# Performance work log

Hardware: AMD Instinct MI355X
Metric: run time of the kernel (lower is better)

The kernel has to match this reference:

```python
import jax, jax.numpy as jnp
import numpy as np

WD, WH, WW = 7, 7, 7  # 3D window size


def _relative_position_index():
    # Matches the torch buffer construction exactly.
    coords = np.stack(np.meshgrid(np.arange(WD), np.arange(WH), np.arange(WW), indexing='ij'))  # [3,wd,wh,ww]
    cf = coords.reshape(3, -1)                      # [3, n]
    rel = cf[:, :, None] - cf[:, None, :]           # [3, n, n]
    rel = rel.transpose(1, 2, 0).copy()             # [n, n, 3]
    rel[..., 0] += WD - 1
    rel[..., 1] += WH - 1
    rel[..., 2] += WW - 1
    rel[..., 0] *= (2 * WH - 1) * (2 * WW - 1)
    rel[..., 1] *= (2 * WW - 1)
    return rel.sum(-1).astype(np.int32)             # [n, n] in [0, 2197)


def setup_inputs() -> dict:
    key = jax.random.key(0)
    ks = jax.random.split(key, 10)
    DIM, H = 192, 6
    B, N, NW = 256, WD * WH * WW, 64  # b = batch*num_windows, NW divides B
    TABLE = (2 * WD - 1) * (2 * WH - 1) * (2 * WW - 1)  # 2197
    w_std = 0.02
    mask = jnp.where(jax.random.uniform(ks[2], (NW, N, N)) < 0.1, -100.0, 0.0).astype(jnp.float32)
    return {
        'x_q': jax.random.normal(ks[0], (B, N, DIM), jnp.float32),
        'x_kv': jax.random.normal(ks[1], (B, N, DIM), jnp.float32),
        'mask': mask,
        'q_w': jax.random.normal(ks[3], (DIM, DIM), jnp.float32) * w_std,
        'q_b': jnp.zeros((DIM,), jnp.float32),
        'kv_w': jax.random.normal(ks[4], (2 * DIM, DIM), jnp.float32) * w_std,
        'kv_b': jnp.zeros((2 * DIM,), jnp.float32),
        'proj_w': jax.random.normal(ks[5], (DIM, DIM), jnp.float32) * w_std,
        'proj_b': jnp.zeros((DIM,), jnp.float32),
        'rpb_table': jax.random.normal(ks[6], (TABLE, H), jnp.float32) * w_std,
        'rpi': jnp.asarray(_relative_position_index()),
    }


def reference(x_q, x_kv, mask, q_w, q_b, kv_w, kv_b, proj_w, proj_b, rpb_table, rpi):
    b, n, c = x_q.shape
    h = rpb_table.shape[-1]
    d = c // h
    scale = d ** (-0.5)
    # projections (torch Linear: y = x @ W.T + b)
    q = (x_q @ q_w.T + q_b).reshape(b, n, h, d)
    kv = x_kv @ kv_w.T + kv_b                      # [b, n, 2c]
    k = kv[..., :c].reshape(b, n, h, d)
    v = kv[..., c:].reshape(b, n, h, d)
    # windowed QK^T
    attn = jnp.einsum('bnhd,bmhd->bhnm', q * scale, k)  # [b, h, n, n]
    # gathered relative-position bias
    rpb = rpb_table[rpi[:n, :n].reshape(-1)].reshape(n, n, h).transpose(2, 0, 1)  # [h, n, n]
    attn = attn + rpb[None]
    # window mask add
    nw = mask.shape[0]
    attn = attn.reshape(b // nw, nw, h, n, n) + mask[None, :, None]
    attn = jax.nn.softmax(attn.reshape(b, h, n, n), axis=-1)
    out = jnp.einsum('bhnm,bmhd->bnhd', attn, v).reshape(b, n, c)
    return out @ proj_w.T + proj_b
```

## Files before the change

kernel.cpp:

```cpp
#include <hip/hip_runtime.h>
#include <hip/hip_bf16.h>
#include <cstdint>

#define B_    256
#define N_    343
#define C_    192
#define H_    6
#define D_    32
#define NW_   64
#define M_    (B_*N_)
#define NN_   (N_*N_)
#define VTS_  352
#define RPS_  344
#define SCALE_ 0.17677669529663687f
#define LOG2E_ 1.4426950408889634f
#define SCALE_LOG2E_ (SCALE_ * LOG2E_)

typedef unsigned short ushort_t;
typedef __attribute__((ext_vector_type(8))) short short8;
typedef __attribute__((ext_vector_type(4))) float f32x4;
typedef __attribute__((ext_vector_type(16))) float f32x16;

__device__ __forceinline__ float b2f(unsigned int u) {
    return __uint_as_float(u << 16);
}
__device__ __forceinline__ unsigned int f2b(float f) {
    unsigned int x = __float_as_uint(f);
    x += 0x7FFFu + ((x >> 16) & 1u);
    return x >> 16;
}
__device__ __forceinline__ unsigned int cvt_pk(float a, float b) {
    unsigned int r;
    asm("v_cvt_pk_bf16_f32 %0, %1, %2" : "=v"(r) : "v"(a), "v"(b));
    return r;
}
__device__ __forceinline__ void pswap(unsigned int &x, unsigned int &y) {
    asm("v_permlane32_swap_b32 %0, %1" : "+v"(x), "+v"(y));
}

__global__ __launch_bounds__(256) void wcvt(
    const float* __restrict__ qw, const float* __restrict__ kvw,
    const float* __restrict__ pw, ushort_t* __restrict__ wb)
{
    int i = blockIdx.x * 256 + threadIdx.x;
    if (i >= 36864) return;
    float4 v;
    if (i < 9216)       v = ((const float4*)qw)[i];
    else if (i < 27648) v = ((const float4*)kvw)[i - 9216];
    else                v = ((const float4*)pw)[i - 27648];
    uint2 u;
    u.x = cvt_pk(v.x, v.y);
    u.y = cvt_pk(v.z, v.w);
    ((uint2*)wb)[i] = u;
}

__global__ __launch_bounds__(512, 4) void gemm_qkv(
    const float* __restrict__ xq, const float* __restrict__ xkv,
    const ushort_t* __restrict__ wb,
    const float* __restrict__ qbias, const float* __restrict__ kvbias,
    ushort_t* __restrict__ qx, ushort_t* __restrict__ kx,
    ushort_t* __restrict__ vtb)
{
    __shared__ ushort_t wls[192 * 200];

    const int t = threadIdx.x, wv = t >> 6, lane = t & 63;
    const int quad = lane >> 4, col = lane & 15;
    const int lid = blockIdx.x;
    const int xcd = lid & 7, idx = lid >> 3;
    const int wg = (xcd < 2 ? xcd * 258 : 2 * 258 + (xcd - 2) * 257) + idx;
    const int jsel = wg % 3;
    const int m0 = (wg / 3) * 128;
    const ushort_t* W = wb + (size_t)jsel * 36864;
    const float* Xf = (jsel == 0) ? xq : xkv;
    const float* bias = (jsel == 0) ? qbias : (jsel == 1 ? kvbias : kvbias + 192);
    const float alpha = (jsel == 0) ? SCALE_LOG2E_ : 1.0f;

    float4 a0[6], a1[6];
    {
        const float* xp = Xf + (size_t)(m0 + wv * 16 + col) * 192;
        #pragma unroll
        for (int kt = 0; kt < 6; ++kt) {
            a0[kt] = *(const float4*)(xp + kt * 32 + quad * 8);
            a1[kt] = *(const float4*)(xp + kt * 32 + quad * 8 + 4);
        }
    }

    for (int c = t; c < 4608; c += 512) {
        int row = c / 24, off = (c % 24) * 8;
        *(short8*)(wls + row * 200 + off) = *(const short8*)(W + row * 192 + off);
    }

    short8 xf[6];
    #pragma unroll
    for (int kt = 0; kt < 6; ++kt) {
        union { short8 s; unsigned int u[4]; } f;
        f.u[0] = cvt_pk(a0[kt].x, a0[kt].y);
        f.u[1] = cvt_pk(a0[kt].z, a0[kt].w);
        f.u[2] = cvt_pk(a1[kt].x, a1[kt].y);
        f.u[3] = cvt_pk(a1[kt].z, a1[kt].w);
        xf[kt] = f.s;
    }
    __syncthreads();

    f32x4 acc[12] = {};
    #pragma unroll
    for (int kt = 0; kt < 6; ++kt)
        #pragma unroll
        for (int ct = 0; ct < 12; ++ct) {
            short8 wf = *(const short8*)(wls + (ct * 16 + col) * 200 + kt * 32 + quad * 8);
            acc[ct] = __builtin_amdgcn_mfma_f32_16x16x32_bf16(wf, xf[kt], acc[ct], 0, 0, 0);
        }

    if (jsel < 2) {
        ushort_t* o16 = (jsel == 0) ? qx : kx;
        int m = m0 + wv * 16 + col;
        int bb = m / N_, nn = m - bb * N_;
        #pragma unroll
        for (int ct = 0; ct < 12; ++ct) {
            float4 bv = *(const float4*)(bias + ct * 16 + quad * 4);
            int hh = ct >> 1;
            int dbase = (ct & 1) * 16 + quad * 4;
            float v0 = (acc[ct][0] + bv.x) * alpha;
            float v1 = (acc[ct][1] + bv.y) * alpha;
            float v2 = (acc[ct][2] + bv.z) * alpha;
            float v3 = (acc[ct][3] + bv.w) * alpha;
            uint2 pk;
            pk.x = cvt_pk(v0, v1);
            pk.y = cvt_pk(v2, v3);
            *(uint2*)(o16 + (((size_t)bb * H_ + hh) * N_ + nn) * D_ + dbase) = pk;
        }
    } else {
        int m = m0 + wv * 16 + col;
        int bb = m / N_, nn = m - bb * N_;
        #pragma unroll
        for (int ct = 0; ct < 12; ++ct) {
            float4 bv = *(const float4*)(bias + ct * 16 + quad * 4);
            int hh = ct >> 1;
            int d0 = (ct & 1) * 16 + quad * 4;
            unsigned int u01 = cvt_pk(acc[ct][0] + bv.x, acc[ct][1] + bv.y);
            unsigned int u23 = cvt_pk(acc[ct][2] + bv.z, acc[ct][3] + bv.w);
            ushort_t* vp = vtb + (((size_t)bb * H_ + hh) * D_ + d0) * VTS_ + nn;
            vp[0]            = (ushort_t)u01;
            vp[VTS_]         = (ushort_t)(u01 >> 16);
            vp[2 * VTS_]     = (ushort_t)u23;
            vp[3 * VTS_]     = (ushort_t)(u23 >> 16);
        }
    }
}

__global__ __launch_bounds__(512, 4) void gemm_out(
    const ushort_t* __restrict__ aob, const ushort_t* __restrict__ wb,
    const float* __restrict__ pbias, float* __restrict__ out)
{
    __shared__ ushort_t wls[192 * 200];

    const int t = threadIdx.x, wv = t >> 6, lane = t & 63;
    const int quad = lane >> 4, col = lane & 15;
    const int m0 = blockIdx.x * 128;
    const ushort_t* W = wb + (size_t)3 * 36864;

    short8 xf[6];
    {
        const ushort_t* xp = aob + (size_t)(m0 + wv * 16 + col) * 192;
        #pragma unroll
        for (int kt = 0; kt < 6; ++kt)
            xf[kt] = *(const short8*)(xp + kt * 32 + quad * 8);
    }
    for (int c = t; c < 4608; c += 512) {
        int row = c / 24, off = (c % 24) * 8;
        *(short8*)(wls + row * 200 + off) = *(const short8*)(W + row * 192 + off);
    }
    __syncthreads();

    f32x4 acc[12] = {};
    #pragma unroll
    for (int kt = 0; kt < 6; ++kt)
        #pragma unroll
        for (int ct = 0; ct < 12; ++ct) {
            short8 wf = *(const short8*)(wls + (ct * 16 + col) * 200 + kt * 32 + quad * 8);
            acc[ct] = __builtin_amdgcn_mfma_f32_16x16x32_bf16(wf, xf[kt], acc[ct], 0, 0, 0);
        }

    int m = m0 + wv * 16 + col;
    #pragma unroll
    for (int ct = 0; ct < 12; ++ct) {
        float4 bv = *(const float4*)(pbias + ct * 16 + quad * 4);
        float4 vo;
        vo.x = acc[ct][0] + bv.x; vo.y = acc[ct][1] + bv.y;
        vo.z = acc[ct][2] + bv.z; vo.w = acc[ct][3] + bv.w;
        *(float4*)(out + (size_t)m * 192 + ct * 16 + quad * 4) = vo;
    }
}

__global__ __launch_bounds__(256) void rpb_gather_b(
    const float* __restrict__ table, const int* __restrict__ rpi,
    ushort_t* __restrict__ rpbb)
{
    int n = blockIdx.x;
    for (int m = threadIdx.x; m < N_; m += 256) {
        int id = rpi[n * N_ + m];
        #pragma unroll
        for (int h = 0; h < H_; ++h)
            rpbb[(size_t)h * (N_ * RPS_) + (size_t)n * RPS_ + m] =
                (ushort_t)f2b(table[(size_t)id * H_ + h] * LOG2E_);
    }
}

__global__ __launch_bounds__(256) void mask_bits(
    const float* __restrict__ mask, unsigned int* __restrict__ mbits)
{
    int gw   = (blockIdx.x * 256 + threadIdx.x) >> 6;
    int lane = threadIdx.x & 63;
    int seg = gw % 6; int rem = gw / 6;
    int n = rem % N_; int w = rem / N_;
    int m = seg * 64 + lane;
    float v = (m < N_) ? mask[((size_t)w * N_ + n) * N_ + m] : -100.f;
    unsigned long long bm = __ballot(v > -50.f);
    if (lane < 2)
        mbits[((size_t)w * N_ + n) * 12 + seg * 2 + lane] = (unsigned int)(bm >> (lane * 32));
}

__global__ __launch_bounds__(256) void vt_pad(ushort_t* __restrict__ vtb)
{
    int bh = blockIdx.x;
    for (int i = threadIdx.x; i < D_ * (VTS_ - N_); i += 256) {
        int d = i / (VTS_ - N_), m = N_ + i % (VTS_ - N_);
        vtb[((size_t)bh * D_ + d) * VTS_ + m] = 0;
    }
}

__global__ __launch_bounds__(256, 5) void attn_mfma(
    const ushort_t* __restrict__ qb, const ushort_t* __restrict__ kb,
    const ushort_t* __restrict__ vtb, const ushort_t* __restrict__ rpbb,
    const unsigned int* __restrict__ mbits, ushort_t* __restrict__ aob)
{
    __shared__ ushort_t ks[352 * 40];

    const int t = threadIdx.x, wv = t >> 6, lane = t & 63;
    const int hh = lane >> 5, c = lane & 31;
    const int lid = blockIdx.x;
    const int wg = (lid & 7) * 576 + (lid >> 3);
    const int qt = wg % 3;
    const int bhx = wg / 3;
    const int h = bhx % H_, b = bhx / H_;
    const int bh = b * H_ + h;
    const int w  = b & (NW_ - 1);
    const int n0 = qt * 128 + wv * 32;

    const ushort_t* kbase = kb + (size_t)bh * (N_ * D_);
    for (int cc = t; cc < (N_ * D_) / 8; cc += 256) {
        int row = cc >> 2, off = (cc & 3) * 8;
        *(short8*)(ks + row * 40 + off) = *(const short8*)(kbase + cc * 8);
    }

    int nn = n0 + c; if (nn > N_ - 1) nn = N_ - 1;
    const ushort_t* qp = qb + ((size_t)bh * N_ + nn) * D_;
    short8 qf0 = *(const short8*)(qp + hh * 8);
    short8 qf1 = *(const short8*)(qp + 16 + hh * 8);

    const unsigned int* mbp = mbits + ((size_t)w * N_ + nn) * 12;
    uint4 mc0 = *(const uint4*)mbp;
    uint4 mc1 = *(const uint4*)(mbp + 4);
    uint4 mc2 = *(const uint4*)(mbp + 8);
    unsigned int dwv[12] = {mc0.x,mc0.y,mc0.z,mc0.w, mc1.x,mc1.y,mc1.z,mc1.w, mc2.x,mc2.y,mc2.z,mc2.w};
    const ushort_t* rpn = rpbb + (size_t)h * (N_ * RPS_) + (size_t)nn * RPS_ + hh * 4;

    __syncthreads();

    const ushort_t* vbase = vtb + (size_t)bh * (D_ * VTS_) + (size_t)c * VTS_;
    f32x16 oacc = {};
    float sum = 0.f;

    #pragma unroll
    for (int kt = 0; kt < 11; ++kt) {
        const ushort_t* krow = ks + (kt * 32 + c) * 40 + hh * 8;
        short8 ka = *(const short8*)(krow);
        short8 kb2 = *(const short8*)(krow + 16);
        f32x16 s = {};
        s = __builtin_amdgcn_mfma_f32_32x32x16_bf16(ka,  qf0, s, 0, 0, 0);
        s = __builtin_amdgcn_mfma_f32_32x32x16_bf16(kb2, qf1, s, 0, 0, 0);

        unsigned int nibs = dwv[kt] >> (hh * 4);
        unsigned int pk[8];
        #pragma unroll
        for (int g = 0; g < 4; ++g) {
            uint2 rv = *(const uint2*)(rpn + kt * 32 + g * 8);
            unsigned int nib = (nibs >> (g * 8)) & 0xFu;
            float e0 = __builtin_exp2f(s[4*g+0] + b2f(rv.x & 0xffffu));
            float e1 = __builtin_exp2f(s[4*g+1] + b2f(rv.x >> 16));
            float e2 = __builtin_exp2f(s[4*g+2] + b2f(rv.y & 0xffffu));
            float e3 = __builtin_exp2f(s[4*g+3] + b2f(rv.y >> 16));
            e0 = (nib & 1u) ? e0 : 0.f;
            e1 = (nib & 2u) ? e1 : 0.f;
            e2 = (nib & 4u) ? e2 : 0.f;
            e3 = (nib & 8u) ? e3 : 0.f;
            sum += (e0 + e1) + (e2 + e3);
            pk[2*g]   = cvt_pk(e0, e1);
            pk[2*g+1] = cvt_pk(e2, e3);
        }
        pswap(pk[0], pk[2]);
        pswap(pk[1], pk[3]);
        pswap(pk[4], pk[6]);
        pswap(pk[5], pk[7]);
        union { short8 s8; unsigned int u[4]; } pf1, pf2;
        pf1.u[0] = pk[0]; pf1.u[1] = pk[1]; pf1.u[2] = pk[2]; pf1.u[3] = pk[3];
        pf2.u[0] = pk[4]; pf2.u[1] = pk[5]; pf2.u[2] = pk[6]; pf2.u[3] = pk[7];

        short8 vf1 = *(const short8*)(vbase + kt * 32 + hh * 8);
        short8 vf2 = *(const short8*)(vbase + kt * 32 + 16 + hh * 8);
        oacc = __builtin_amdgcn_mfma_f32_32x32x16_bf16(vf1, pf1.s8, oacc, 0, 0, 0);
        oacc = __builtin_amdgcn_mfma_f32_32x32x16_bf16(vf2, pf2.s8, oacc, 0, 0, 0);
    }

    sum += __shfl_xor(sum, 32);

    int n = n0 + c;
    if (n < N_) {
        float inv = 1.0f / sum;
        ushort_t* op = aob + ((size_t)b * N_ + n) * C_ + h * D_ + hh * 4;
        #pragma unroll
        for (int g = 0; g < 4; ++g) {
            uint2 pkk;
            pkk.x = cvt_pk(oacc[4*g+0] * inv, oacc[4*g+1] * inv);
            pkk.y = cvt_pk(oacc[4*g+2] * inv, oacc[4*g+3] * inv);
            *(uint2*)(op + g * 8) = pkk;
        }
    }
}

extern "C" void kernel_launch(void* const* d_in, const int* in_sizes, int n_in,
                              void* d_out, int out_size, void* d_ws, size_t ws_size,
                              hipStream_t stream)
{
    const float* x_q    = (const float*)d_in[0];
    const float* x_kv   = (const float*)d_in[1];
    const float* mask   = (const float*)d_in[2];
    const float* q_w    = (const float*)d_in[3];
    const float* q_b    = (const float*)d_in[4];
    const float* kv_w   = (const float*)d_in[5];
    const float* kv_b   = (const float*)d_in[6];
    const float* proj_w = (const float*)d_in[7];
    const float* proj_b = (const float*)d_in[8];
    const float* rpb_t  = (const float*)d_in[9];
    const int*   rpi    = (const int*)d_in[10];
    float* out = (float*)d_out;

    const size_t QKV  = (size_t)B_ * H_ * N_ * D_;
    const size_t QKV2 = (size_t)B_ * H_ * D_ * VTS_;
    char* ws = (char*)d_ws;
    ushort_t* qx   = (ushort_t*)ws;
    ushort_t* kx   = qx + QKV;
    ushort_t* vtb  = kx + QKV;
    ushort_t* aob  = vtb + QKV2;
    ushort_t* rpbb = aob + QKV;
    ushort_t* wb   = rpbb + ((size_t)H_ * N_ * RPS_ + 16);
    unsigned int* mbits = (unsigned int*)(wb + 147456);

    wcvt<<<144, 256, 0, stream>>>(q_w, kv_w, proj_w, wb);
    rpb_gather_b<<<N_, 256, 0, stream>>>(rpb_t, rpi, rpbb);
    mask_bits<<<(NW_ * N_ * 6) / 4, 256, 0, stream>>>(mask, mbits);
    vt_pad<<<B_ * H_, 256, 0, stream>>>(vtb);
    gemm_qkv<<<2058, 512, 0, stream>>>(
        x_q, x_kv, wb, q_b, kv_b, qx, kx, vtb);
    attn_mfma<<<4608, 256, 0, stream>>>(qx, kx, vtb, rpbb, mbits, aob);
    gemm_out<<<M_/128, 512, 0, stream>>>(aob, wb, proj_b, out);
}
```

Before: 394.4 us.

## Stage V in LDS and transpose bias/mask tables for coalesced per-row loads

The attention kernel now copies each head's transposed V tile into shared memory once per workgroup and reads MFMA V fragments from LDS instead of global memory. The relative-position bias and mask-bit tables are re-laid out so that adjacent query rows are contiguous, which makes lane reads of bias quads and mask words coalesced. The mask_bits kernel is restructured to one wave per row. The extra LDS lowers the occupancy hint from 5 to 3 blocks per CU, trading latency hiding for fewer scattered global loads.

```diff
diff --git a/kernel.cpp b/kernel.cpp
--- a/kernel.cpp
+++ b/kernel.cpp
@@ -11,7 +11,8 @@
 #define M_    (B_*N_)
 #define NN_   (N_*N_)
 #define VTS_  352
-#define RPS_  344
+#define VLS_  360
+#define RPG_  86
 #define SCALE_ 0.17677669529663687f
 #define LOG2E_ 1.4426950408889634f
 #define SCALE_LOG2E_ (SCALE_ * LOG2E_)
@@ -194,30 +195,36 @@
 
 __global__ __launch_bounds__(256) void rpb_gather_b(
     const float* __restrict__ table, const int* __restrict__ rpi,
-    ushort_t* __restrict__ rpbb)
+    ushort_t* __restrict__ rpbt)
 {
     int n = blockIdx.x;
     for (int m = threadIdx.x; m < N_; m += 256) {
         int id = rpi[n * N_ + m];
+        int mg = m >> 2, mi = m & 3;
         #pragma unroll
         for (int h = 0; h < H_; ++h)
-            rpbb[(size_t)h * (N_ * RPS_) + (size_t)n * RPS_ + m] =
+            rpbt[((((size_t)h * RPG_ + mg) * N_) + n) * 4 + mi] =
                 (ushort_t)f2b(table[(size_t)id * H_ + h] * LOG2E_);
     }
 }
 
 __global__ __launch_bounds__(256) void mask_bits(
-    const float* __restrict__ mask, unsigned int* __restrict__ mbits)
-{
-    int gw   = (blockIdx.x * 256 + threadIdx.x) >> 6;
+    const float* __restrict__ mask, unsigned int* __restrict__ mbt)
+{
+    int gw   = blockIdx.x * 4 + (threadIdx.x >> 6);
     int lane = threadIdx.x & 63;
-    int seg = gw % 6; int rem = gw / 6;
-    int n = rem % N_; int w = rem / N_;
-    int m = seg * 64 + lane;
-    float v = (m < N_) ? mask[((size_t)w * N_ + n) * N_ + m] : -100.f;
-    unsigned long long bm = __ballot(v > -50.f);
-    if (lane < 2)
-        mbits[((size_t)w * N_ + n) * 12 + seg * 2 + lane] = (unsigned int)(bm >> (lane * 32));
+    int n = gw % N_, w = gw / N_;
+    if (w >= NW_) return;
+    const float* mrow = mask + ((size_t)w * N_ + n) * N_;
+    #pragma unroll
+    for (int seg = 0; seg < 6; ++seg) {
+        int m = seg * 64 + lane;
+        float v = (m < N_) ? mrow[m] : -100.f;
+        unsigned long long bm = __ballot(v > -50.f);
+        if (lane < 2)
+            mbt[((size_t)w * 12 + seg * 2 + lane) * N_ + n] =
+                (unsigned int)(bm >> (lane * 32));
+    }
 }
 
 __global__ __launch_bounds__(256) void vt_pad(ushort_t* __restrict__ vtb)
@@ -229,12 +236,13 @@
     }
 }
 
-__global__ __launch_bounds__(256, 5) void attn_mfma(
+__global__ __launch_bounds__(256, 3) void attn_mfma(
     const ushort_t* __restrict__ qb, const ushort_t* __restrict__ kb,
-    const ushort_t* __restrict__ vtb, const ushort_t* __restrict__ rpbb,
-    const unsigned int* __restrict__ mbits, ushort_t* __restrict__ aob)
+    const ushort_t* __restrict__ vtb, const ushort_t* __restrict__ rpbt,
+    const unsigned int* __restrict__ mbt, ushort_t* __restrict__ aob)
 {
     __shared__ ushort_t ks[352 * 40];
+    __shared__ ushort_t vls[32 * VLS_];
 
     const int t = threadIdx.x, wv = t >> 6, lane = t & 63;
     const int hh = lane >> 5, c = lane & 31;
@@ -252,29 +260,34 @@
         int row = cc >> 2, off = (cc & 3) * 8;
         *(short8*)(ks + row * 40 + off) = *(const short8*)(kbase + cc * 8);
     }
+    const ushort_t* vbase = vtb + (size_t)bh * (D_ * VTS_);
+    for (int cc = t; cc < (D_ * VTS_) / 8; cc += 256) {
+        int row = cc / 44, off = (cc % 44) * 8;
+        *(short8*)(vls + row * VLS_ + off) = *(const short8*)(vbase + cc * 8);
+    }
 
     int nn = n0 + c; if (nn > N_ - 1) nn = N_ - 1;
     const ushort_t* qp = qb + ((size_t)bh * N_ + nn) * D_;
     short8 qf0 = *(const short8*)(qp + hh * 8);
     short8 qf1 = *(const short8*)(qp + 16 + hh * 8);
 
-    const unsigned int* mbp = mbits + ((size_t)w * N_ + nn) * 12;
-    uint4 mc0 = *(const uint4*)mbp;
-    uint4 mc1 = *(const uint4*)(mbp + 4);
-    uint4 mc2 = *(const uint4*)(mbp + 8);
-    unsigned int dwv[12] = {mc0.x,mc0.y,mc0.z,mc0.w, mc1.x,mc1.y,mc1.z,mc1.w, mc2.x,mc2.y,mc2.z,mc2.w};
-    const ushort_t* rpn = rpbb + (size_t)h * (N_ * RPS_) + (size_t)nn * RPS_ + hh * 4;
+    unsigned int dwv[12];
+    {
+        const unsigned int* mbp = mbt + (size_t)w * 12 * N_ + nn;
+        #pragma unroll
+        for (int i = 0; i < 12; ++i) dwv[i] = mbp[i * N_];
+    }
+    const uint2* rp2 = (const uint2*)rpbt + (size_t)h * (RPG_ * N_) + nn;
 
     __syncthreads();
 
-    const ushort_t* vbase = vtb + (size_t)bh * (D_ * VTS_) + (size_t)c * VTS_;
     f32x16 oacc = {};
     float sum = 0.f;
 
     #pragma unroll
     for (int kt = 0; kt < 11; ++kt) {
         const ushort_t* krow = ks + (kt * 32 + c) * 40 + hh * 8;
-        short8 ka = *(const short8*)(krow);
+        short8 ka  = *(const short8*)(krow);
         short8 kb2 = *(const short8*)(krow + 16);
         f32x16 s = {};
         s = __builtin_amdgcn_mfma_f32_32x32x16_bf16(ka,  qf0, s, 0, 0, 0);
@@ -284,7 +297,9 @@
         unsigned int pk[8];
         #pragma unroll
         for (int g = 0; g < 4; ++g) {
-            uint2 rv = *(const uint2*)(rpn + kt * 32 + g * 8);
+            int mg = kt * 8 + 2 * g + hh;
+            if (mg > RPG_ - 1) mg = RPG_ - 1;
+            uint2 rv = rp2[(size_t)mg * N_];
             unsigned int nib = (nibs >> (g * 8)) & 0xFu;
             float e0 = __builtin_exp2f(s[4*g+0] + b2f(rv.x & 0xffffu));
             float e1 = __builtin_exp2f(s[4*g+1] + b2f(rv.x >> 16));
@@ -306,8 +321,9 @@
         pf1.u[0] = pk[0]; pf1.u[1] = pk[1]; pf1.u[2] = pk[2]; pf1.u[3] = pk[3];
         pf2.u[0] = pk[4]; pf2.u[1] = pk[5]; pf2.u[2] = pk[6]; pf2.u[3] = pk[7];
 
-        short8 vf1 = *(const short8*)(vbase + kt * 32 + hh * 8);
-        short8 vf2 = *(const short8*)(vbase + kt * 32 + 16 + hh * 8);
+        const ushort_t* vrow = vls + c * VLS_ + kt * 32 + hh * 8;
+        short8 vf1 = *(const short8*)(vrow);
+        short8 vf2 = *(const short8*)(vrow + 16);
         oacc = __builtin_amdgcn_mfma_f32_32x32x16_bf16(vf1, pf1.s8, oacc, 0, 0, 0);
         oacc = __builtin_amdgcn_mfma_f32_32x32x16_bf16(vf2, pf2.s8, oacc, 0, 0, 0);
     }
@@ -352,16 +368,16 @@
     ushort_t* kx   = qx + QKV;
     ushort_t* vtb  = kx + QKV;
     ushort_t* aob  = vtb + QKV2;
-    ushort_t* rpbb = aob + QKV;
-    ushort_t* wb   = rpbb + ((size_t)H_ * N_ * RPS_ + 16);
-    unsigned int* mbits = (unsigned int*)(wb + 147456);
+    ushort_t* rpbt = aob + QKV;
+    ushort_t* wb   = rpbt + (size_t)H_ * RPG_ * N_ * 4;
+    unsigned int* mbt = (unsigned int*)(wb + 147456);
 
     wcvt<<<144, 256, 0, stream>>>(q_w, kv_w, proj_w, wb);
-    rpb_gather_b<<<N_, 256, 0, stream>>>(rpb_t, rpi, rpbb);
-    mask_bits<<<(NW_ * N_ * 6) / 4, 256, 0, stream>>>(mask, mbits);
+    rpb_gather_b<<<N_, 256, 0, stream>>>(rpb_t, rpi, rpbt);
+    mask_bits<<<(NW_ * N_) / 4, 256, 0, stream>>>(mask, mbt);
     vt_pad<<<B_ * H_, 256, 0, stream>>>(vtb);
     gemm_qkv<<<2058, 512, 0, stream>>>(
         x_q, x_kv, wb, q_b, kv_b, qx, kx, vtb);
-    attn_mfma<<<4608, 256, 0, stream>>>(qx, kx, vtb, rpbb, mbits, aob);
+    attn_mfma<<<4608, 256, 0, stream>>>(qx, kx, vtb, rpbt, mbt, aob);
     gemm_out<<<M_/128, 512, 0, stream>>>(aob, wb, proj_b, out);
 }
```

Result: faster. 383.1 us (-2.9%).
